# Optimization experiments

Hardware: AMD Instinct MI355X
Metric: run time of the kernel (lower is better)

## Reference

```python
import jax, jax.numpy as jnp
import numpy as np

N = 40000      # num atoms
E = 640000     # num edges (avg degree 16)
H = 128        # hidden_channels
R = 64         # num_rbf
NB = 3         # num interaction blocks
CUT = 5.0      # cutoff_upper
NT = 100       # num atom types (embedding rows)


def setup_inputs() -> dict:
    key = jax.random.key(0)
    ks = jax.random.split(key, 24)

    def lin_w(k, fan_in, fan_out):
        # xavier-uniform-like scale
        lim = np.sqrt(6.0 / (fan_in + fan_out)).astype(np.float32)
        return jax.random.uniform(k, (fan_in, fan_out), jnp.float32, -lim, lim)

    def stack_w(k, fan_in, fan_out):
        kk = jax.random.split(k, NB)
        return jnp.stack([lin_w(kk[i], fan_in, fan_out) for i in range(NB)])

    inp = {}
    inp["atom_types"] = jax.random.randint(ks[0], (N,), 0, NT)
    inp["edge_index"] = jax.random.randint(ks[1], (2, E), 0, N)
    inp["edge_weight"] = jax.random.uniform(ks[2], (E,), jnp.float32) * CUT

    inp["emb"] = jax.random.normal(ks[3], (NT, H), jnp.float32) * 0.1
    # CFConv params per block (stacked on leading NB axis)
    inp["lin1_w"] = stack_w(ks[4], H, H)            # no bias
    inp["fw1"] = stack_w(ks[5], R, H)
    inp["fb1"] = jnp.zeros((NB, H), jnp.float32)
    inp["fw2"] = stack_w(ks[6], H, H)
    inp["fb2"] = jnp.zeros((NB, H), jnp.float32)
    inp["lin2_w"] = stack_w(ks[7], H, H)
    inp["lin2_b"] = jnp.zeros((NB, H), jnp.float32)
    # InteractionBlock trailing linear
    inp["lin_w"] = stack_w(ks[8], H, H)
    inp["lin_b"] = jnp.zeros((NB, H), jnp.float32)
    # output network: H -> H//2 -> 1
    inp["o1_w"] = lin_w(ks[9], H, H // 2)
    inp["o1_b"] = jnp.zeros((H // 2,), jnp.float32)
    inp["o2_w"] = lin_w(ks[10], H // 2, 1)
    inp["o2_b"] = jnp.zeros((1,), jnp.float32)
    return inp


def _schnet_fwd(atom_types, edge_index, edge_weight, emb, lin1_w, fw1, fb1,
                fw2, fb2, lin2_w, lin2_b, lin_w, lin_b, o1_w, o1_b, o2_w, o2_b):
    # Gaussian RBF expansion of distances: (E, R)
    offsets = jnp.linspace(0.0, CUT, R).astype(edge_weight.dtype)
    coeff = -0.5 / (offsets[1] - offsets[0]) ** 2
    rbf = jnp.exp(coeff * (edge_weight[:, None] - offsets[None, :]) ** 2)
    # cosine cutoff envelope: (E,)
    C = 0.5 * (jnp.cos(jnp.pi * edge_weight / CUT) + 1.0)
    C = C * (edge_weight < CUT).astype(edge_weight.dtype)

    src = edge_index[0]
    dst = edge_index[1]

    x = emb[atom_types]  # (N, H)
    for b in range(NB):
        # filter network on expanded distances: (E, H)
        W = jnp.tanh(rbf @ fw1[b] + fb1[b]) @ fw2[b] + fb2[b]
        W = W * C[:, None]
        # CFConv: project, gather by src, modulate, scatter-sum to dst
        h = x @ lin1_w[b]                              # (N, H)
        msg = h[src] * W                               # (E, H)
        agg = jax.ops.segment_sum(msg, dst, num_segments=N)  # (N, H)
        y = agg @ lin2_w[b] + lin2_b[b]
        # InteractionBlock tail: activation then linear; residual in SchNet
        y = jnp.tanh(y) @ lin_w[b] + lin_b[b]
        x = x + y
    # output network: per-atom scalar energies (N, 1)
    energy = jnp.tanh(x @ o1_w + o1_b) @ o2_w + o2_b
    return energy


def reference(atom_types, edge_index, edge_weight, emb, lin1_w, fw1, fb1,
              fw2, fb2, lin2_w, lin2_b, lin_w, lin_b, o1_w, o1_b, o2_w, o2_b):
    return _schnet_fwd(atom_types, edge_index, edge_weight, emb, lin1_w, fw1,
                       fb1, fw2, fb2, lin2_w, lin2_b, lin_w, lin_b, o1_w,
                       o1_b, o2_w, o2_b)
```

## Files before the change

### kernel.cpp

```cpp
#include <hip/hip_runtime.h>
#include <math.h>

#define N_ATOMS 40000
#define E_EDGES 640000
#define H 128
#define RBF 64
#define NBLK 3
#define CUTF 5.0f
#define TBL 4096

__device__ __forceinline__ float fast_tanh(float x) {
    return 1.0f - 2.0f / (1.0f + __expf(2.0f * x));
}

__global__ __launch_bounds__(256) void k_embed(const int* __restrict__ types,
                                               const float* __restrict__ emb,
                                               float* __restrict__ x) {
    int flat4 = blockIdx.x * 256 + threadIdx.x;
    int i = flat4 >> 5;
    int c4 = flat4 & 31;
    int t = types[i];
    const float4* e4 = (const float4*)(emb + (size_t)t * H);
    ((float4*)(x + (size_t)i * H))[c4] = e4[c4];
}

__global__ __launch_bounds__(256) void k_count(const int* __restrict__ eidx,
                                               int* __restrict__ cnt) {
    int e = blockIdx.x * 256 + threadIdx.x;
    atomicAdd(&cnt[eidx[E_EDGES + e]], 1);
}

__global__ __launch_bounds__(1024) void k_scanA(const int* __restrict__ cnt,
                                                int* __restrict__ bsum) {
    __shared__ int ws[16];
    const int tid = threadIdx.x, lane = tid & 63, wid = tid >> 6;
    int idx = blockIdx.x * 1024 + tid;
    int v = (idx < N_ATOMS) ? cnt[idx] : 0;
#pragma unroll
    for (int off = 32; off; off >>= 1) v += __shfl_xor(v, off, 64);
    if (lane == 0) ws[wid] = v;
    __syncthreads();
    if (tid == 0) {
        int s = 0;
#pragma unroll
        for (int w = 0; w < 16; ++w) s += ws[w];
        bsum[blockIdx.x] = s;
    }
}

__global__ __launch_bounds__(64) void k_scanB(const int* __restrict__ bsum,
                                              int* __restrict__ boff) {
    const int lane = threadIdx.x;
    int v = (lane < 40) ? bsum[lane] : 0;
    int inc = v;
#pragma unroll
    for (int off = 1; off < 64; off <<= 1) {
        int t = __shfl_up(inc, off, 64);
        if (lane >= off) inc += t;
    }
    if (lane < 40) boff[lane] = inc - v;
}

__global__ __launch_bounds__(1024) void k_scanC(const int* __restrict__ cnt,
                                                const int* __restrict__ boff,
                                                int* __restrict__ cursor,
                                                int* __restrict__ rstart) {
    __shared__ int wsum[16];
    __shared__ int woff[16];
    const int tid = threadIdx.x, lane = tid & 63, wid = tid >> 6;
    int idx = blockIdx.x * 1024 + tid;
    int v = (idx < N_ATOMS) ? cnt[idx] : 0;
    int inc = v;
#pragma unroll
    for (int off = 1; off < 64; off <<= 1) {
        int t = __shfl_up(inc, off, 64);
        if (lane >= off) inc += t;
    }
    if (lane == 63) wsum[wid] = inc;
    __syncthreads();
    if (tid == 0) {
        int acc = 0;
#pragma unroll
        for (int w = 0; w < 16; ++w) { woff[w] = acc; acc += wsum[w]; }
    }
    __syncthreads();
    if (idx < N_ATOMS) {
        int ex = boff[blockIdx.x] + woff[wid] + inc - v;
        cursor[idx] = ex;
        rstart[idx] = ex;
    }
}

__global__ __launch_bounds__(256) void k_fill(const int* __restrict__ eidx,
                                              const float* __restrict__ ew,
                                              int* __restrict__ cursor,
                                              int2* __restrict__ pmeta) {
    int e = blockIdx.x * 256 + threadIdx.x;
    int dd = eidx[E_EDGES + e];
    int pos = atomicAdd(&cursor[dd], 1);
    float u = ew[e] * ((float)(TBL - 1) / CUTF);
    pmeta[pos] = make_int2(eidx[e], __float_as_int(u));
}

__global__ __launch_bounds__(256, 2) void k_table(const float* __restrict__ fw1all,
                                                  const float* __restrict__ fb1all,
                                                  const float* __restrict__ fw2all,
                                                  const float* __restrict__ fb2all,
                                                  float* __restrict__ tab) {
    const int b = blockIdx.y;
    const float* fw1 = fw1all + (size_t)b * RBF * H;
    const float* fb1 = fb1all + (size_t)b * H;
    const float* fw2 = fw2all + (size_t)b * H * H;
    const float* fb2 = fb2all + (size_t)b * H;
    float* tabB = tab + (size_t)b * TBL * H;

    __shared__ float tile[128 * 133];
    const int tid = threadIdx.x;
    const int mbase = blockIdx.x * 128;
    const float DSTEP = CUTF / (float)(TBL - 1);

    {
        const int e = tid & 127;
        const int k0 = (tid >> 7) * 32;
        const float d = (float)(mbase + e) * DSTEP;
        const float DELTA = CUTF / 63.0f;
        const float COEFF = -0.5f / (DELTA * DELTA);
#pragma unroll
        for (int k = k0; k < k0 + 32; ++k) {
            float diff = d - (float)k * DELTA;
            tile[e * 133 + k] = __expf(COEFF * diff * diff);
        }
    }
    __syncthreads();

    const int eg = tid >> 4, cg = tid & 15;
    const int e0 = eg * 8, c0 = cg * 8;

    float acc[8][8];
#pragma unroll
    for (int i = 0; i < 8; ++i)
#pragma unroll
        for (int j = 0; j < 8; ++j) acc[i][j] = 0.0f;

#pragma unroll 4
    for (int k = 0; k < RBF; ++k) {
        float a[8];
#pragma unroll
        for (int i = 0; i < 8; ++i) a[i] = tile[(e0 + i) * 133 + k];
        const float4 b0 = *(const float4*)(fw1 + (size_t)k * H + c0);
        const float4 b1 = *(const float4*)(fw1 + (size_t)k * H + c0 + 4);
        const float bb[8] = {b0.x, b0.y, b0.z, b0.w, b1.x, b1.y, b1.z, b1.w};
#pragma unroll
        for (int i = 0; i < 8; ++i)
#pragma unroll
            for (int j = 0; j < 8; ++j) acc[i][j] = fmaf(a[i], bb[j], acc[i][j]);
    }

    {
        const float4 q0 = *(const float4*)(fb1 + c0);
        const float4 q1 = *(const float4*)(fb1 + c0 + 4);
        const float bv[8] = {q0.x, q0.y, q0.z, q0.w, q1.x, q1.y, q1.z, q1.w};
#pragma unroll
        for (int i = 0; i < 8; ++i)
#pragma unroll
            for (int j = 0; j < 8; ++j) acc[i][j] = fast_tanh(acc[i][j] + bv[j]);
    }

    __syncthreads();
#pragma unroll
    for (int i = 0; i < 8; ++i)
#pragma unroll
        for (int j = 0; j < 8; ++j) tile[(e0 + i) * 133 + c0 + j] = acc[i][j];
    __syncthreads();

#pragma unroll
    for (int i = 0; i < 8; ++i)
#pragma unroll
        for (int j = 0; j < 8; ++j) acc[i][j] = 0.0f;

#pragma unroll 4
    for (int k = 0; k < H; ++k) {
        float a[8];
#pragma unroll
        for (int i = 0; i < 8; ++i) a[i] = tile[(e0 + i) * 133 + k];
        const float4 b0 = *(const float4*)(fw2 + (size_t)k * H + c0);
        const float4 b1 = *(const float4*)(fw2 + (size_t)k * H + c0 + 4);
        const float bb[8] = {b0.x, b0.y, b0.z, b0.w, b1.x, b1.y, b1.z, b1.w};
#pragma unroll
        for (int i = 0; i < 8; ++i)
#pragma unroll
            for (int j = 0; j < 8; ++j) acc[i][j] = fmaf(a[i], bb[j], acc[i][j]);
    }

    const float4 q0 = *(const float4*)(fb2 + c0);
    const float4 q1 = *(const float4*)(fb2 + c0 + 4);
    const float bv[8] = {q0.x, q0.y, q0.z, q0.w, q1.x, q1.y, q1.z, q1.w};

#pragma unroll
    for (int ei = 0; ei < 8; ++ei) {
        const int m = mbase + e0 + ei;
        const float d = (float)m * DSTEP;
        float c = 0.5f * (cosf(0.6283185307179586f * d) + 1.0f);
        c = (d < CUTF) ? c : 0.0f;
        float* op = tabB + (size_t)m * H + c0;
        float r[8];
#pragma unroll
        for (int j = 0; j < 8; ++j) r[j] = (acc[ei][j] + bv[j]) * c;
        *(float4*)(op)     = make_float4(r[0], r[1], r[2], r[3]);
        *(float4*)(op + 4) = make_float4(r[4], r[5], r[6], r[7]);
    }
}

__global__ __launch_bounds__(128, 2) void k_gemm_nh(const float* __restrict__ A,
                                                    const float* __restrict__ W,
                                                    float* __restrict__ out) {
    __shared__ float at[64 * 133];
    const int tid = threadIdx.x;
    const int abase = blockIdx.x * 64;

#pragma unroll
    for (int i = 0; i < 16; ++i) {
        int flat4 = tid + 128 * i;
        int r = flat4 >> 5, k4 = flat4 & 31;
        float4 v = ((const float4*)(A + (size_t)(abase + r) * H))[k4];
        float* dp = &at[r * 133 + k4 * 4];
        dp[0] = v.x; dp[1] = v.y; dp[2] = v.z; dp[3] = v.w;
    }
    __syncthreads();

    const int eg = tid >> 4, cg = tid & 15;
    const int e0 = eg * 8, c0 = cg * 8;

    float acc[8][8];
#pragma unroll
    for (int i = 0; i < 8; ++i)
#pragma unroll
        for (int j = 0; j < 8; ++j) acc[i][j] = 0.0f;

#pragma unroll 4
    for (int k = 0; k < H; ++k) {
        float a[8];
#pragma unroll
        for (int i = 0; i < 8; ++i) a[i] = at[(e0 + i) * 133 + k];
        const float4 b0 = *(const float4*)(W + (size_t)k * H + c0);
        const float4 b1 = *(const float4*)(W + (size_t)k * H + c0 + 4);
        const float bb[8] = {b0.x, b0.y, b0.z, b0.w, b1.x, b1.y, b1.z, b1.w};
#pragma unroll
        for (int i = 0; i < 8; ++i)
#pragma unroll
            for (int j = 0; j < 8; ++j) acc[i][j] = fmaf(a[i], bb[j], acc[i][j]);
    }

#pragma unroll
    for (int ei = 0; ei < 8; ++ei) {
        const int row = abase + e0 + ei;
        float* op = out + (size_t)row * H + c0;
        *(float4*)(op)     = make_float4(acc[ei][0], acc[ei][1], acc[ei][2], acc[ei][3]);
        *(float4*)(op + 4) = make_float4(acc[ei][4], acc[ei][5], acc[ei][6], acc[ei][7]);
    }
}

template <bool MAKE_H>
__global__ __launch_bounds__(128, 2) void k_tail(const float* __restrict__ agg,
                                                 const float* __restrict__ lin2,
                                                 const float* __restrict__ b2,
                                                 const float* __restrict__ linw,
                                                 const float* __restrict__ bl,
                                                 float* __restrict__ x,
                                                 const float* __restrict__ lin1n,
                                                 float* __restrict__ hout) {
    __shared__ float at[64 * 133];
    const int tid = threadIdx.x;
    const int abase = blockIdx.x * 64;

#pragma unroll
    for (int i = 0; i < 16; ++i) {
        int flat4 = tid + 128 * i;
        int r = flat4 >> 5, k4 = flat4 & 31;
        float4 v = ((const float4*)(agg + (size_t)(abase + r) * H))[k4];
        float* dp = &at[r * 133 + k4 * 4];
        dp[0] = v.x; dp[1] = v.y; dp[2] = v.z; dp[3] = v.w;
    }
    __syncthreads();

    const int eg = tid >> 4, cg = tid & 15;
    const int e0 = eg * 8, c0 = cg * 8;

    float acc[8][8];
#pragma unroll
    for (int i = 0; i < 8; ++i)
#pragma unroll
        for (int j = 0; j < 8; ++j) acc[i][j] = 0.0f;

#pragma unroll 4
    for (int k = 0; k < H; ++k) {
        float a[8];
#pragma unroll
        for (int i = 0; i < 8; ++i) a[i] = at[(e0 + i) * 133 + k];
        const float4 b0 = *(const float4*)(lin2 + (size_t)k * H + c0);
        const float4 b1 = *(const float4*)(lin2 + (size_t)k * H + c0 + 4);
        const float bb[8] = {b0.x, b0.y, b0.z, b0.w, b1.x, b1.y, b1.z, b1.w};
#pragma unroll
        for (int i = 0; i < 8; ++i)
#pragma unroll
            for (int j = 0; j < 8; ++j) acc[i][j] = fmaf(a[i], bb[j], acc[i][j]);
    }
    {
        const float4 q0 = *(const float4*)(b2 + c0);
        const float4 q1 = *(const float4*)(b2 + c0 + 4);
        const float bv[8] = {q0.x, q0.y, q0.z, q0.w, q1.x, q1.y, q1.z, q1.w};
#pragma unroll
        for (int i = 0; i < 8; ++i)
#pragma unroll
            for (int j = 0; j < 8; ++j) acc[i][j] = fast_tanh(acc[i][j] + bv[j]);
    }

    __syncthreads();
#pragma unroll
    for (int i = 0; i < 8; ++i)
#pragma unroll
        for (int j = 0; j < 8; ++j) at[(e0 + i) * 133 + c0 + j] = acc[i][j];
    __syncthreads();

#pragma unroll
    for (int i = 0; i < 8; ++i)
#pragma unroll
        for (int j = 0; j < 8; ++j) acc[i][j] = 0.0f;

#pragma unroll 4
    for (int k = 0; k < H; ++k) {
        float a[8];
#pragma unroll
        for (int i = 0; i < 8; ++i) a[i] = at[(e0 + i) * 133 + k];
        const float4 b0 = *(const float4*)(linw + (size_t)k * H + c0);
        const float4 b1 = *(const float4*)(linw + (size_t)k * H + c0 + 4);
        const float bb[8] = {b0.x, b0.y, b0.z, b0.w, b1.x, b1.y, b1.z, b1.w};
#pragma unroll
        for (int i = 0; i < 8; ++i)
#pragma unroll
            for (int j = 0; j < 8; ++j) acc[i][j] = fmaf(a[i], bb[j], acc[i][j]);
    }

    {
        const float4 q0 = *(const float4*)(bl + c0);
        const float4 q1 = *(const float4*)(bl + c0 + 4);
        const float bv[8] = {q0.x, q0.y, q0.z, q0.w, q1.x, q1.y, q1.z, q1.w};
        if (MAKE_H) __syncthreads();
#pragma unroll
        for (int ei = 0; ei < 8; ++ei) {
            const int row = abase + e0 + ei;
            float* op = x + (size_t)row * H + c0;
            float4 x0 = *(const float4*)(op);
            float4 x1 = *(const float4*)(op + 4);
            float xn[8] = {x0.x + acc[ei][0] + bv[0], x0.y + acc[ei][1] + bv[1],
                           x0.z + acc[ei][2] + bv[2], x0.w + acc[ei][3] + bv[3],
                           x1.x + acc[ei][4] + bv[4], x1.y + acc[ei][5] + bv[5],
                           x1.z + acc[ei][6] + bv[6], x1.w + acc[ei][7] + bv[7]};
            *(float4*)(op)     = make_float4(xn[0], xn[1], xn[2], xn[3]);
            *(float4*)(op + 4) = make_float4(xn[4], xn[5], xn[6], xn[7]);
            if (MAKE_H) {
#pragma unroll
                for (int j = 0; j < 8; ++j) at[(e0 + ei) * 133 + c0 + j] = xn[j];
            }
        }
    }

    if (MAKE_H) {
        __syncthreads();
#pragma unroll
        for (int i = 0; i < 8; ++i)
#pragma unroll
            for (int j = 0; j < 8; ++j) acc[i][j] = 0.0f;

#pragma unroll 4
        for (int k = 0; k < H; ++k) {
            float a[8];
#pragma unroll
            for (int i = 0; i < 8; ++i) a[i] = at[(e0 + i) * 133 + k];
            const float4 b0 = *(const float4*)(lin1n + (size_t)k * H + c0);
            const float4 b1 = *(const float4*)(lin1n + (size_t)k * H + c0 + 4);
            const float bb[8] = {b0.x, b0.y, b0.z, b0.w, b1.x, b1.y, b1.z, b1.w};
#pragma unroll
            for (int i = 0; i < 8; ++i)
#pragma unroll
                for (int j = 0; j < 8; ++j) acc[i][j] = fmaf(a[i], bb[j], acc[i][j]);
        }

#pragma unroll
        for (int ei = 0; ei < 8; ++ei) {
            const int row = abase + e0 + ei;
            float* op = hout + (size_t)row * H + c0;
            *(float4*)(op)     = make_float4(acc[ei][0], acc[ei][1], acc[ei][2], acc[ei][3]);
            *(float4*)(op + 4) = make_float4(acc[ei][4], acc[ei][5], acc[ei][6], acc[ei][7]);
        }
    }
}

__global__ __launch_bounds__(256) void k_edge4(const int* __restrict__ rstart,
                                               const int* __restrict__ rend,
                                               const int2* __restrict__ pmeta,
                                               const float* __restrict__ tab,
                                               const float* __restrict__ h,
                                               float* __restrict__ agg) {
    const int wave = threadIdx.x >> 6;
    const int lane = threadIdx.x & 63;
    const int a = blockIdx.x * 4 + wave;
    const int col0 = lane * 2;

    const int s = rstart[a];
    const int n = rend[a] - s;

    float s0 = 0.0f, s1 = 0.0f;
    if (n <= 64) {
        int2 meta = make_int2(0, 0);
        if (lane < n) meta = pmeta[s + lane];
#pragma unroll 2
        for (int e = 0; e < n; ++e) {
            const int src = __shfl(meta.x, e, 64);
            const float u = __int_as_float(__shfl(meta.y, e, 64));
            int i0 = (int)u;
            i0 = (i0 > TBL - 2) ? (TBL - 2) : i0;
            const float f = u - (float)i0;
            const float2 lo = *(const float2*)(tab + (size_t)i0 * H + col0);
            const float2 hi = *(const float2*)(tab + ((size_t)i0 + 1) * H + col0);
            const float2 hv = *(const float2*)(h + (size_t)src * H + col0);
            s0 = fmaf(fmaf(f, hi.x - lo.x, lo.x), hv.x, s0);
            s1 = fmaf(fmaf(f, hi.y - lo.y, lo.y), hv.y, s1);
        }
    } else {
        for (int e = s; e < s + n; ++e) {
            const int2 m = pmeta[e];
            const float u = __int_as_float(m.y);
            int i0 = (int)u;
            i0 = (i0 > TBL - 2) ? (TBL - 2) : i0;
            const float f = u - (float)i0;
            const float2 lo = *(const float2*)(tab + (size_t)i0 * H + col0);
            const float2 hi = *(const float2*)(tab + ((size_t)i0 + 1) * H + col0);
            const float2 hv = *(const float2*)(h + (size_t)m.x * H + col0);
            s0 = fmaf(fmaf(f, hi.x - lo.x, lo.x), hv.x, s0);
            s1 = fmaf(fmaf(f, hi.y - lo.y, lo.y), hv.y, s1);
        }
    }
    *(float2*)(agg + (size_t)a * H + col0) = make_float2(s0, s1);
}

__global__ __launch_bounds__(256) void k_out(const float* __restrict__ x,
                                             const float* __restrict__ o1w,
                                             const float* __restrict__ o1b,
                                             const float* __restrict__ o2w,
                                             const float* __restrict__ o2b,
                                             float* __restrict__ out) {
    __shared__ float xs[64 * 132];
    const int tid = threadIdx.x;
    const int abase = blockIdx.x * 64;

#pragma unroll
    for (int i = 0; i < 8; ++i) {
        int flat4 = tid + 256 * i;
        int r = flat4 >> 5, k4 = flat4 & 31;
        float4 v = ((const float4*)(x + (size_t)(abase + r) * H))[k4];
        float* dp = &xs[r * 132 + k4 * 4];
        dp[0] = v.x; dp[1] = v.y; dp[2] = v.z; dp[3] = v.w;
    }
    __syncthreads();

    const int eg = tid >> 4, cg = tid & 15;
    const int r0 = eg * 4, c0 = cg * 4;

    float acc[4][4];
#pragma unroll
    for (int i = 0; i < 4; ++i)
#pragma unroll
        for (int j = 0; j < 4; ++j) acc[i][j] = 0.0f;

#pragma unroll 4
    for (int k = 0; k < H; ++k) {
        float a[4];
#pragma unroll
        for (int i = 0; i < 4; ++i) a[i] = xs[(r0 + i) * 132 + k];
        const float4 b = *(const float4*)(o1w + (size_t)k * 64 + c0);
        const float bb[4] = {b.x, b.y, b.z, b.w};
#pragma unroll
        for (int i = 0; i < 4; ++i)
#pragma unroll
            for (int j = 0; j < 4; ++j) acc[i][j] = fmaf(a[i], bb[j], acc[i][j]);
    }

    const float4 ob = *(const float4*)(o1b + c0);
    const float4 ow = *(const float4*)(o2w + c0);
    const float obv[4] = {ob.x, ob.y, ob.z, ob.w};
    const float owv[4] = {ow.x, ow.y, ow.z, ow.w};
    float p[4];
#pragma unroll
    for (int i = 0; i < 4; ++i) {
        float s = 0.0f;
#pragma unroll
        for (int j = 0; j < 4; ++j) s = fmaf(fast_tanh(acc[i][j] + obv[j]), owv[j], s);
        p[i] = s;
    }
#pragma unroll
    for (int off = 1; off < 16; off <<= 1) {
#pragma unroll
        for (int i = 0; i < 4; ++i) p[i] += __shfl_xor(p[i], off, 64);
    }
    if (cg == 0) {
        const float b2 = o2b[0];
#pragma unroll
        for (int i = 0; i < 4; ++i) out[abase + r0 + i] = p[i] + b2;
    }
}

extern "C" void kernel_launch(void* const* d_in, const int* in_sizes, int n_in,
                              void* d_out, int out_size, void* d_ws, size_t ws_size,
                              hipStream_t stream) {
    const int*   types = (const int*)d_in[0];
    const int*   eidx  = (const int*)d_in[1];
    const float* ew    = (const float*)d_in[2];
    const float* emb   = (const float*)d_in[3];
    const float* lin1  = (const float*)d_in[4];
    const float* fw1   = (const float*)d_in[5];
    const float* fb1   = (const float*)d_in[6];
    const float* fw2   = (const float*)d_in[7];
    const float* fb2   = (const float*)d_in[8];
    const float* lin2  = (const float*)d_in[9];
    const float* lin2b = (const float*)d_in[10];
    const float* linw  = (const float*)d_in[11];
    const float* linb  = (const float*)d_in[12];
    const float* o1w   = (const float*)d_in[13];
    const float* o1b   = (const float*)d_in[14];
    const float* o2w   = (const float*)d_in[15];
    const float* o2b   = (const float*)d_in[16];
    float* out = (float*)d_out;

    float* x      = (float*)d_ws;
    float* h      = x + (size_t)N_ATOMS * H;
    float* agg    = h + (size_t)N_ATOMS * H;
    float* tab    = agg + (size_t)N_ATOMS * H;
    int*   cnt    = (int*)(tab + (size_t)NBLK * TBL * H);
    int*   cursor = cnt + N_ATOMS;
    int*   rstart = cursor + N_ATOMS;
    int*   bsum   = rstart + N_ATOMS;
    int*   boff   = bsum + 64;
    int2*  pmeta  = (int2*)(boff + 64);

    hipMemsetAsync(cnt, 0, N_ATOMS * sizeof(int), stream);
    k_count<<<E_EDGES / 256, 256, 0, stream>>>(eidx, cnt);
    k_scanA<<<40, 1024, 0, stream>>>(cnt, bsum);
    k_scanB<<<1, 64, 0, stream>>>(bsum, boff);
    k_scanC<<<40, 1024, 0, stream>>>(cnt, boff, cursor, rstart);
    k_fill<<<E_EDGES / 256, 256, 0, stream>>>(eidx, ew, cursor, pmeta);

    k_embed<<<(N_ATOMS * H / 4) / 256, 256, 0, stream>>>(types, emb, x);
    k_table<<<dim3(TBL / 128, NBLK), 256, 0, stream>>>(fw1, fb1, fw2, fb2, tab);

    k_gemm_nh<<<N_ATOMS / 64, 128, 0, stream>>>(x, lin1, h);

    for (int b = 0; b < NBLK; ++b) {
        k_edge4<<<N_ATOMS / 4, 256, 0, stream>>>(rstart, cursor, pmeta,
                                                 tab + (size_t)b * TBL * H, h, agg);
        if (b < NBLK - 1) {
            k_tail<true><<<N_ATOMS / 64, 128, 0, stream>>>(
                agg, lin2 + (size_t)b * H * H, lin2b + (size_t)b * H,
                linw + (size_t)b * H * H, linb + (size_t)b * H, x,
                lin1 + (size_t)(b + 1) * H * H, h);
        } else {
            k_tail<false><<<N_ATOMS / 64, 128, 0, stream>>>(
                agg, lin2 + (size_t)b * H * H, lin2b + (size_t)b * H,
                linw + (size_t)b * H * H, linb + (size_t)b * H, x,
                nullptr, nullptr);
        }
    }

    k_out<<<N_ATOMS / 64, 256, 0, stream>>>(x, o1w, o1b, o2w, o2b, out);
}
```

Baseline: 665.0 us.

## Precompute embedding times lin1 per atom type and retile tail kernel

Since x starts as emb[atom_types], h = x @ lin1[0] equals (emb @ lin1[0])[atom_types]. A tiny 100x128 GEMM replaces the full N x H GEMM, and the embed kernel now gathers both x and h. Separately, the fused tail kernel moves to 256 threads with 4x8 register tiles per thread instead of 8x8, lowering register pressure to raise occupancy at the cost of more shared-memory reads per FMA.

```diff
diff --git a/kernel.cpp b/kernel.cpp
--- a/kernel.cpp
+++ b/kernel.cpp
@@ -13,15 +13,28 @@
     return 1.0f - 2.0f / (1.0f + __expf(2.0f * x));
 }
 
-__global__ __launch_bounds__(256) void k_embed(const int* __restrict__ types,
-                                               const float* __restrict__ emb,
-                                               float* __restrict__ x) {
+__global__ __launch_bounds__(128) void k_embw(const float* __restrict__ emb,
+                                              const float* __restrict__ lin1,
+                                              float* __restrict__ embw) {
+    const int t = blockIdx.x;
+    const int c = threadIdx.x;
+    float s = 0.0f;
+#pragma unroll 8
+    for (int k = 0; k < H; ++k) s = fmaf(emb[t * H + k], lin1[(size_t)k * H + c], s);
+    embw[t * H + c] = s;
+}
+
+__global__ __launch_bounds__(256) void k_embed2(const int* __restrict__ types,
+                                                const float* __restrict__ emb,
+                                                const float* __restrict__ embw,
+                                                float* __restrict__ x,
+                                                float* __restrict__ h) {
     int flat4 = blockIdx.x * 256 + threadIdx.x;
     int i = flat4 >> 5;
     int c4 = flat4 & 31;
     int t = types[i];
-    const float4* e4 = (const float4*)(emb + (size_t)t * H);
-    ((float4*)(x + (size_t)i * H))[c4] = e4[c4];
+    ((float4*)(x + (size_t)i * H))[c4] = ((const float4*)(emb + (size_t)t * H))[c4];
+    ((float4*)(h + (size_t)i * H))[c4] = ((const float4*)(embw + (size_t)t * H))[c4];
 }
 
 __global__ __launch_bounds__(256) void k_count(const int* __restrict__ eidx,
@@ -211,71 +224,22 @@
     }
 }
 
-__global__ __launch_bounds__(128, 2) void k_gemm_nh(const float* __restrict__ A,
-                                                    const float* __restrict__ W,
-                                                    float* __restrict__ out) {
+template <bool MAKE_H>
+__global__ __launch_bounds__(256) void k_tail(const float* __restrict__ agg,
+                                              const float* __restrict__ lin2,
+                                              const float* __restrict__ b2,
+                                              const float* __restrict__ linw,
+                                              const float* __restrict__ bl,
+                                              float* __restrict__ x,
+                                              const float* __restrict__ lin1n,
+                                              float* __restrict__ hout) {
     __shared__ float at[64 * 133];
     const int tid = threadIdx.x;
     const int abase = blockIdx.x * 64;
 
 #pragma unroll
-    for (int i = 0; i < 16; ++i) {
-        int flat4 = tid + 128 * i;
-        int r = flat4 >> 5, k4 = flat4 & 31;
-        float4 v = ((const float4*)(A + (size_t)(abase + r) * H))[k4];
-        float* dp = &at[r * 133 + k4 * 4];
-        dp[0] = v.x; dp[1] = v.y; dp[2] = v.z; dp[3] = v.w;
-    }
-    __syncthreads();
-
-    const int eg = tid >> 4, cg = tid & 15;
-    const int e0 = eg * 8, c0 = cg * 8;
-
-    float acc[8][8];
-#pragma unroll
-    for (int i = 0; i < 8; ++i)
-#pragma unroll
-        for (int j = 0; j < 8; ++j) acc[i][j] = 0.0f;
-
-#pragma unroll 4
-    for (int k = 0; k < H; ++k) {
-        float a[8];
-#pragma unroll
-        for (int i = 0; i < 8; ++i) a[i] = at[(e0 + i) * 133 + k];
-        const float4 b0 = *(const float4*)(W + (size_t)k * H + c0);
-        const float4 b1 = *(const float4*)(W + (size_t)k * H + c0 + 4);
-        const float bb[8] = {b0.x, b0.y, b0.z, b0.w, b1.x, b1.y, b1.z, b1.w};
-#pragma unroll
-        for (int i = 0; i < 8; ++i)
-#pragma unroll
-            for (int j = 0; j < 8; ++j) acc[i][j] = fmaf(a[i], bb[j], acc[i][j]);
-    }
-
-#pragma unroll
-    for (int ei = 0; ei < 8; ++ei) {
-        const int row = abase + e0 + ei;
-        float* op = out + (size_t)row * H + c0;
-        *(float4*)(op)     = make_float4(acc[ei][0], acc[ei][1], acc[ei][2], acc[ei][3]);
-        *(float4*)(op + 4) = make_float4(acc[ei][4], acc[ei][5], acc[ei][6], acc[ei][7]);
-    }
-}
-
-template <bool MAKE_H>
-__global__ __launch_bounds__(128, 2) void k_tail(const float* __restrict__ agg,
-                                                 const float* __restrict__ lin2,
-                                                 const float* __restrict__ b2,
-                                                 const float* __restrict__ linw,
-                                                 const float* __restrict__ bl,
-                                                 float* __restrict__ x,
-                                                 const float* __restrict__ lin1n,
-                                                 float* __restrict__ hout) {
-    __shared__ float at[64 * 133];
-    const int tid = threadIdx.x;
-    const int abase = blockIdx.x * 64;
-
-#pragma unroll
-    for (int i = 0; i < 16; ++i) {
-        int flat4 = tid + 128 * i;
+    for (int i = 0; i < 8; ++i) {
+        int flat4 = tid + 256 * i;
         int r = flat4 >> 5, k4 = flat4 & 31;
         float4 v = ((const float4*)(agg + (size_t)(abase + r) * H))[k4];
         float* dp = &at[r * 133 + k4 * 4];
@@ -284,24 +248,24 @@
     __syncthreads();
 
     const int eg = tid >> 4, cg = tid & 15;
-    const int e0 = eg * 8, c0 = cg * 8;
-
-    float acc[8][8];
-#pragma unroll
-    for (int i = 0; i < 8; ++i)
+    const int r0 = eg * 4, c0 = cg * 8;
+
+    float acc[4][8];
+#pragma unroll
+    for (int i = 0; i < 4; ++i)
 #pragma unroll
         for (int j = 0; j < 8; ++j) acc[i][j] = 0.0f;
 
 #pragma unroll 4
     for (int k = 0; k < H; ++k) {
-        float a[8];
-#pragma unroll
-        for (int i = 0; i < 8; ++i) a[i] = at[(e0 + i) * 133 + k];
+        float a[4];
+#pragma unroll
+        for (int i = 0; i < 4; ++i) a[i] = at[(r0 + i) * 133 + k];
         const float4 b0 = *(const float4*)(lin2 + (size_t)k * H + c0);
         const float4 b1 = *(const float4*)(lin2 + (size_t)k * H + c0 + 4);
         const float bb[8] = {b0.x, b0.y, b0.z, b0.w, b1.x, b1.y, b1.z, b1.w};
 #pragma unroll
-        for (int i = 0; i < 8; ++i)
+        for (int i = 0; i < 4; ++i)
 #pragma unroll
             for (int j = 0; j < 8; ++j) acc[i][j] = fmaf(a[i], bb[j], acc[i][j]);
     }
@@ -310,33 +274,33 @@
         const float4 q1 = *(const float4*)(b2 + c0 + 4);
         const float bv[8] = {q0.x, q0.y, q0.z, q0.w, q1.x, q1.y, q1.z, q1.w};
 #pragma unroll
-        for (int i = 0; i < 8; ++i)
+        for (int i = 0; i < 4; ++i)
 #pragma unroll
             for (int j = 0; j < 8; ++j) acc[i][j] = fast_tanh(acc[i][j] + bv[j]);
     }
 
     __syncthreads();
 #pragma unroll
-    for (int i = 0; i < 8; ++i)
-#pragma unroll
-        for (int j = 0; j < 8; ++j) at[(e0 + i) * 133 + c0 + j] = acc[i][j];
-    __syncthreads();
-
-#pragma unroll
-    for (int i = 0; i < 8; ++i)
+    for (int i = 0; i < 4; ++i)
+#pragma unroll
+        for (int j = 0; j < 8; ++j) at[(r0 + i) * 133 + c0 + j] = acc[i][j];
+    __syncthreads();
+
+#pragma unroll
+    for (int i = 0; i < 4; ++i)
 #pragma unroll
         for (int j = 0; j < 8; ++j) acc[i][j] = 0.0f;
 
 #pragma unroll 4
     for (int k = 0; k < H; ++k) {
-        float a[8];
-#pragma unroll
-        for (int i = 0; i < 8; ++i) a[i] = at[(e0 + i) * 133 + k];
+        float a[4];
+#pragma unroll
+        for (int i = 0; i < 4; ++i) a[i] = at[(r0 + i) * 133 + k];
         const float4 b0 = *(const float4*)(linw + (size_t)k * H + c0);
         const float4 b1 = *(const float4*)(linw + (size_t)k * H + c0 + 4);
         const float bb[8] = {b0.x, b0.y, b0.z, b0.w, b1.x, b1.y, b1.z, b1.w};
 #pragma unroll
-        for (int i = 0; i < 8; ++i)
+        for (int i = 0; i < 4; ++i)
 #pragma unroll
             for (int j = 0; j < 8; ++j) acc[i][j] = fmaf(a[i], bb[j], acc[i][j]);
     }
@@ -347,8 +311,8 @@
         const float bv[8] = {q0.x, q0.y, q0.z, q0.w, q1.x, q1.y, q1.z, q1.w};
         if (MAKE_H) __syncthreads();
 #pragma unroll
-        for (int ei = 0; ei < 8; ++ei) {
-            const int row = abase + e0 + ei;
+        for (int ei = 0; ei < 4; ++ei) {
+            const int row = abase + r0 + ei;
             float* op = x + (size_t)row * H + c0;
             float4 x0 = *(const float4*)(op);
             float4 x1 = *(const float4*)(op + 4);
@@ -360,38 +324,39 @@
             *(float4*)(op + 4) = make_float4(xn[4], xn[5], xn[6], xn[7]);
             if (MAKE_H) {
 #pragma unroll
-                for (int j = 0; j < 8; ++j) at[(e0 + ei) * 133 + c0 + j] = xn[j];
+                for (int j = 0; j < 8; ++j) at[(r0 + ei) * 133 + c0 + j] = xn[j];
             }
         }
     }
 
     if (MAKE_H) {
         __syncthreads();
-#pragma unroll
-        for (int i = 0; i < 8; ++i)
-#pragma unroll
-            for (int j = 0; j < 8; ++j) acc[i][j] = 0.0f;
+        float acc3[4][8];
+#pragma unroll
+        for (int i = 0; i < 4; ++i)
+#pragma unroll
+            for (int j = 0; j < 8; ++j) acc3[i][j] = 0.0f;
 
 #pragma unroll 4
         for (int k = 0; k < H; ++k) {
-            float a[8];
-#pragma unroll
-            for (int i = 0; i < 8; ++i) a[i] = at[(e0 + i) * 133 + k];
+            float a[4];
+#pragma unroll
+            for (int i = 0; i < 4; ++i) a[i] = at[(r0 + i) * 133 + k];
             const float4 b0 = *(const float4*)(lin1n + (size_t)k * H + c0);
             const float4 b1 = *(const float4*)(lin1n + (size_t)k * H + c0 + 4);
             const float bb[8] = {b0.x, b0.y, b0.z, b0.w, b1.x, b1.y, b1.z, b1.w};
 #pragma unroll
-            for (int i = 0; i < 8; ++i)
-#pragma unroll
-                for (int j = 0; j < 8; ++j) acc[i][j] = fmaf(a[i], bb[j], acc[i][j]);
-        }
-
-#pragma unroll
-        for (int ei = 0; ei < 8; ++ei) {
-            const int row = abase + e0 + ei;
+            for (int i = 0; i < 4; ++i)
+#pragma unroll
+                for (int j = 0; j < 8; ++j) acc3[i][j] = fmaf(a[i], bb[j], acc3[i][j]);
+        }
+
+#pragma unroll
+        for (int ei = 0; ei < 4; ++ei) {
+            const int row = abase + r0 + ei;
             float* op = hout + (size_t)row * H + c0;
-            *(float4*)(op)     = make_float4(acc[ei][0], acc[ei][1], acc[ei][2], acc[ei][3]);
-            *(float4*)(op + 4) = make_float4(acc[ei][4], acc[ei][5], acc[ei][6], acc[ei][7]);
+            *(float4*)(op)     = make_float4(acc3[ei][0], acc3[ei][1], acc3[ei][2], acc3[ei][3]);
+            *(float4*)(op + 4) = make_float4(acc3[ei][4], acc3[ei][5], acc3[ei][6], acc3[ei][7]);
         }
     }
 }
@@ -536,7 +501,8 @@
     float* h      = x + (size_t)N_ATOMS * H;
     float* agg    = h + (size_t)N_ATOMS * H;
     float* tab    = agg + (size_t)N_ATOMS * H;
-    int*   cnt    = (int*)(tab + (size_t)NBLK * TBL * H);
+    float* embw   = tab + (size_t)NBLK * TBL * H;
+    int*   cnt    = (int*)(embw + 100 * H);
     int*   cursor = cnt + N_ATOMS;
     int*   rstart = cursor + N_ATOMS;
     int*   bsum   = rstart + N_ATOMS;
@@ -550,21 +516,20 @@
     k_scanC<<<40, 1024, 0, stream>>>(cnt, boff, cursor, rstart);
     k_fill<<<E_EDGES / 256, 256, 0, stream>>>(eidx, ew, cursor, pmeta);
 
-    k_embed<<<(N_ATOMS * H / 4) / 256, 256, 0, stream>>>(types, emb, x);
+    k_embw<<<100, 128, 0, stream>>>(emb, lin1, embw);
+    k_embed2<<<(N_ATOMS * H / 4) / 256, 256, 0, stream>>>(types, emb, embw, x, h);
     k_table<<<dim3(TBL / 128, NBLK), 256, 0, stream>>>(fw1, fb1, fw2, fb2, tab);
-
-    k_gemm_nh<<<N_ATOMS / 64, 128, 0, stream>>>(x, lin1, h);
 
     for (int b = 0; b < NBLK; ++b) {
         k_edge4<<<N_ATOMS / 4, 256, 0, stream>>>(rstart, cursor, pmeta,
                                                  tab + (size_t)b * TBL * H, h, agg);
         if (b < NBLK - 1) {
-            k_tail<true><<<N_ATOMS / 64, 128, 0, stream>>>(
+            k_tail<true><<<N_ATOMS / 64, 256, 0, stream>>>(
                 agg, lin2 + (size_t)b * H * H, lin2b + (size_t)b * H,
                 linw + (size_t)b * H * H, linb + (size_t)b * H, x,
                 lin1 + (size_t)(b + 1) * H * H, h);
         } else {
-            k_tail<false><<<N_ATOMS / 64, 128, 0, stream>>>(
+            k_tail<false><<<N_ATOMS / 64, 256, 0, stream>>>(
                 agg, lin2 + (size_t)b * H * H, lin2b + (size_t)b * H,
                 linw + (size_t)b * H * H, linb + (size_t)b * H, x,
                 nullptr, nullptr);
```

Result: faster. 639.4 us (-3.9%).
